# Kernel tuning notes

Measured on AMD Instinct MI355X. Metric: run time of the kernel, lower is better.

The kernel has to match this reference:

```python
import jax, jax.numpy as jnp
import numpy as np

D_MODEL = 1024
NUM_HEADS = 16
HEAD_DIM = D_MODEL // NUM_HEADS
THETA = 10000.0
MAX_SEQ_LEN = 2048
BATCH = 4
SEQ = 2048


def _rope_tables():
    # theta_vec = 1 / theta**(arange(0, d_k, 2)/d_k), pos outer product
    inv_freq = 1.0 / (THETA ** (jnp.arange(0, HEAD_DIM, 2, dtype=jnp.float32) / HEAD_DIM))
    pos = jnp.arange(MAX_SEQ_LEN, dtype=jnp.float32)
    freqs = jnp.outer(pos, inv_freq)  # [max_seq, head_dim//2]
    return jnp.cos(freqs), jnp.sin(freqs)


def apply_rope(x, cos, sin):
    # x: [..., S, d]; cos/sin: [S, d//2]; interleaved pairwise rotation
    x1 = x[..., 0::2]
    x2 = x[..., 1::2]
    o1 = x1 * cos - x2 * sin
    o2 = x2 * cos + x1 * sin
    return jnp.stack([o1, o2], axis=-1).reshape(x.shape)


def setup_inputs() -> dict:
    key = jax.random.key(0)
    kx, kq, kk, kv, ko = jax.random.split(key, 5)
    std = (1.0 / D_MODEL) ** 0.5
    x = jax.random.normal(kx, (BATCH, SEQ, D_MODEL), dtype=jnp.float32)
    w_q = jax.random.normal(kq, (D_MODEL, D_MODEL), dtype=jnp.float32) * std
    w_k = jax.random.normal(kk, (D_MODEL, D_MODEL), dtype=jnp.float32) * std
    w_v = jax.random.normal(kv, (D_MODEL, D_MODEL), dtype=jnp.float32) * std
    w_o = jax.random.normal(ko, (D_MODEL, D_MODEL), dtype=jnp.float32) * std
    cos, sin = _rope_tables()
    return {"x": x, "w_q": w_q, "w_k": w_k, "w_v": w_v, "w_o": w_o,
            "cos": cos, "sin": sin}


def reference(x, w_q, w_k, w_v, w_o, cos, sin):
    b, s, d = x.shape
    h, dk = NUM_HEADS, HEAD_DIM

    def proj(w):
        # einsum '... s d, hd d -> ... s hd' == x @ w.T, then split heads
        y = jnp.einsum('bsd,ed->bse', x, w)
        return y.reshape(b, s, h, dk).transpose(0, 2, 1, 3)  # [b,h,s,dk]

    q = apply_rope(proj(w_q), cos[:s], sin[:s])
    k = apply_rope(proj(w_k), cos[:s], sin[:s])
    v = proj(w_v)

    scores = jnp.einsum('bhnd,bhmd->bhnm', q, k) / (dk ** 0.5)
    causal = jnp.tril(jnp.ones((s, s), dtype=bool))
    scores = jnp.where(causal, scores, -jnp.inf)
    attn = jax.nn.softmax(scores, axis=-1)
    out = jnp.einsum('bhnm,bhmd->bhnd', attn, v)  # [b,h,s,dk]
    out = out.transpose(0, 2, 1, 3).reshape(b, s, d)
    # einsum '... s hd, d hd -> ... s d' == out @ w_o.T
    return jnp.einsum('bse,de->bsd', out, w_o)
```

## Files before the change

### kernel.cpp

```cpp
#include <hip/hip_runtime.h>
#include <hip/hip_bf16.h>


typedef __bf16 bf16;
typedef __bf16 bf16x8 __attribute__((ext_vector_type(8)));
typedef __bf16 bf16x4 __attribute__((ext_vector_type(4)));
typedef float f32x4 __attribute__((ext_vector_type(4)));

#define LOG2E 1.4426950408889634f
#define QSCALE (0.125f * LOG2E * 8388608.0f)
#define SEXP_SEED ((126.94269504f - 16.0f * LOG2E) * 8388608.0f)

__device__ __forceinline__ void async16(const void* g, void* l) {
  __builtin_amdgcn_global_load_lds(
      (const __attribute__((address_space(1))) void*)g,
      (__attribute__((address_space(3))) void*)l, 16, 0, 0);
}

#define MFMA16(a, b, c) __builtin_amdgcn_mfma_f32_16x16x32_bf16(a, b, c, 0, 0, 0)

__global__ void cast_all_kernel(const float* __restrict__ x,
                                const float* __restrict__ wq,
                                const float* __restrict__ wk,
                                const float* __restrict__ wv,
                                const float* __restrict__ wo,
                                const float* __restrict__ cosT,
                                const float* __restrict__ sinT,
                                bf16* __restrict__ xb, bf16* __restrict__ wb,
                                float2* __restrict__ csT) {
  int i = blockIdx.x * blockDim.x + threadIdx.x;
  if (i >= 3145728) {
    int j = i - 3145728;
    float2 cs;
    cs.x = cosT[j];
    cs.y = sinT[j];
    csT[j] = cs;
    return;
  }
  const float* src;
  bf16* dst;
  long o;
  if (i < 2097152) {
    src = x; dst = xb; o = i;
  } else {
    long j = i - 2097152;
    int w = (int)(j >> 18);
    o = j & 262143;
    src = (w == 0) ? wq : (w == 1) ? wk : (w == 2) ? wv : wo;
    dst = wb + (long)w * 1048576;
  }
  float4 v = reinterpret_cast<const float4*>(src)[o];
  bf16x4 out;
  out.x = (bf16)v.x; out.y = (bf16)v.y; out.z = (bf16)v.z; out.w = (bf16)v.w;
  *reinterpret_cast<bf16x4*>(dst + o * 4) = out;
}

template <int EPI, int TM, int TN>
__device__ __forceinline__ void gemm_dev(const bf16* __restrict__ A,
                                         const bf16* __restrict__ B,
                                         void* __restrict__ C, int N, int K,
                                         int bm, int bn, bf16* As, bf16* Bs,
                                         const float2* __restrict__ csT) {
  constexpr int WM = TM / 64;
  constexpr int WN = 4 / WM;
  constexpr int CW = TN / WN;
  constexpr int NT = CW / 16;
  constexpr int ROUNDS = (TM + TN) / 32;
  const int tid = threadIdx.x;
  const int wid = tid >> 6, lane = tid & 63;
  const int quad = lane >> 4, l15 = lane & 15;
  const int waveM = wid / WN, waveN = wid % WN;

  f32x4 acc[4][NT] = {};
  const bf16* Ag = A + (long)bm * TM * K;
  const bf16* Bg = B + (long)bn * TN * K;

  for (int k0 = 0; k0 < K; k0 += 64) {
#pragma unroll
    for (int ri = 0; ri < ROUNDS; ++ri) {
      int ci = ri * 256 + tid;
      int gb = ri * 256 + (wid << 6);
      bool isA = gb < TM * 8;
      int cl = isA ? ci : ci - TM * 8;
      int r = cl >> 3;
      int col = ((cl & 7) ^ (r & 7)) << 3;
      const bf16* src = (isA ? Ag : Bg) + (long)r * K + k0 + col;
      char* dst = isA ? ((char*)As + (long)ci * 16)
                      : ((char*)Bs + (long)(ci - TM * 8) * 16);
      async16(src, dst);
    }
    __syncthreads();
#pragma unroll
    for (int kk = 0; kk < 2; ++kk) {
      bf16x8 af[4], bfr[NT];
#pragma unroll
      for (int t = 0; t < 4; ++t) {
        int rowA = waveM * 64 + t * 16 + l15;
        af[t] = *(const bf16x8*)(As + rowA * 64 +
                                 ((((kk << 2) + quad) ^ (rowA & 7)) << 3));
      }
#pragma unroll
      for (int t = 0; t < NT; ++t) {
        int rowB = waveN * CW + t * 16 + l15;
        bfr[t] = *(const bf16x8*)(Bs + rowB * 64 +
                                  ((((kk << 2) + quad) ^ (rowB & 7)) << 3));
      }
#pragma unroll
      for (int mt = 0; mt < 4; ++mt)
#pragma unroll
        for (int nt = 0; nt < NT; ++nt)
          acc[mt][nt] = MFMA16(af[mt], bfr[nt], acc[mt][nt]);
    }
    if (k0 + 64 < K) __syncthreads();
  }

  const float qsc = (EPI == 0 && bn < 8) ? QSCALE : 1.0f;
#pragma unroll
  for (int mt = 0; mt < 4; ++mt)
#pragma unroll
    for (int nt = 0; nt < NT; ++nt)
#pragma unroll
      for (int r = 0; r < 4; ++r) {
        int row = bm * TM + waveM * 64 + mt * 16 + quad * 4 + r;
        int col = bn * TN + waveN * CW + nt * 16 + l15;
        float v = acc[mt][nt][r];
        if (EPI == 0) {
          float pr = __shfl_xor(v, 1);
          int d = col & 63;
          float2 cs = csT[(row & 2047) * 32 + (d >> 1)];
          float o =
              (col & 1) ? (v * cs.x + pr * cs.y) : (v * cs.x - pr * cs.y);
          o *= qsc;
          long off = (long)(col >> 10) * 8388608 +
                     (long)(((row >> 11) << 4) + ((col >> 6) & 15)) * 131072 +
                     (long)(row & 2047) * 64 + d;
          ((bf16*)C)[off] = (bf16)o;
        } else if (EPI == 1) {
          long off = (long)(col >> 11) * 2097152 + (long)row * 2048 +
                     (col & 2047);
          ((bf16*)C)[off] = (bf16)v;
        } else {
          ((float*)C)[(long)row * N + col] = v;
        }
      }
}

__global__ __launch_bounds__(256) void gemm_qkv(const bf16* __restrict__ xb,
                                                const bf16* __restrict__ wqk,
                                                const bf16* __restrict__ wv,
                                                bf16* __restrict__ QK,
                                                bf16* __restrict__ VT,
                                                const float2* __restrict__ csT) {
  __shared__ __align__(16) bf16 As[128 * 64];
  __shared__ __align__(16) bf16 Bs[128 * 64];
  int p = blockIdx.x;
  if (p >= 1024) {
    int pv = p - 1024;
    int lv = (pv & 7) * 64 + (pv >> 3);
    gemm_dev<1, 128, 128>(wv, xb, VT, 8192, 1024, lv & 7, lv >> 3, As, Bs,
                          nullptr);
  } else {
    int l = (p & 7) * 128 + (p >> 3);
    gemm_dev<0, 128, 128>(xb, wqk, QK, 2048, 1024, l >> 4, l & 15, As, Bs,
                          csT);
  }
}

__global__ __launch_bounds__(256) void gemm_out(const bf16* __restrict__ A,
                                                const bf16* __restrict__ B,
                                                float* __restrict__ C) {
  __shared__ __align__(16) bf16 As[128 * 64];
  __shared__ __align__(16) bf16 Bs[128 * 64];
  int p = blockIdx.x;
  int l = (p & 7) * 64 + (p >> 3);
  gemm_dev<2, 128, 128>(A, B, C, 1024, 1024, l >> 3, l & 7, As, Bs, nullptr);
}

__device__ __forceinline__ void attn_step(const bf16* Ks, const bf16* Vs,
                                          bf16* Pw, const bf16x8* qf,
                                          const bf16x8 ones, f32x4* accO,
                                          f32x4& accL, int quad, int l15,
                                          int qloc, bool diag) {
  const int sw = l15 & 7;
  const f32x4 seedv = {SEXP_SEED, SEXP_SEED, SEXP_SEED, SEXP_SEED};
  f32x4 sacc[4] = {seedv, seedv, seedv, seedv};
#pragma unroll
  for (int mt = 0; mt < 4; ++mt)
#pragma unroll
    for (int kk = 0; kk < 2; ++kk) {
      bf16x8 kf = *(const bf16x8*)(Ks + (mt * 16 + l15) * 64 +
                                   ((((kk << 2) + quad) ^ sw) << 3));
      sacc[mt] = MFMA16(kf, qf[kk], sacc[mt]);
    }
  if (diag) {
#pragma unroll
    for (int mt = 0; mt < 4; ++mt)
#pragma unroll
      for (int r = 0; r < 4; ++r)
        if ((mt * 16 + quad * 4 + r) > qloc) sacc[mt][r] = 0.0f;
  }
#pragma unroll
  for (int mt = 0; mt < 4; ++mt) {
    int i0 = (int)sacc[mt][0], i1 = (int)sacc[mt][1];
    int i2 = (int)sacc[mt][2], i3 = (int)sacc[mt][3];
    uint2 pk;
    pk.x = __builtin_amdgcn_perm((unsigned)i1, (unsigned)i0, 0x07060302u);
    pk.y = __builtin_amdgcn_perm((unsigned)i3, (unsigned)i2, 0x07060302u);
    *(uint2*)(Pw + l15 * 88 + mt * 16 + quad * 4) = pk;
  }
  asm volatile("s_waitcnt lgkmcnt(0)" ::: "memory");
  bf16x8 pfr[2];
#pragma unroll
  for (int kk = 0; kk < 2; ++kk)
    pfr[kk] = *(const bf16x8*)(Pw + l15 * 88 + kk * 32 + quad * 8);
#pragma unroll
  for (int nt = 0; nt < 4; ++nt)
#pragma unroll
    for (int kk = 0; kk < 2; ++kk) {
      bf16x8 vf = *(const bf16x8*)(Vs + (nt * 16 + l15) * 64 +
                                   ((((kk << 2) + quad) ^ sw) << 3));
      accO[nt] = MFMA16(pfr[kk], vf, accO[nt]);
    }
#pragma unroll
  for (int kk = 0; kk < 2; ++kk)
    accL = MFMA16(pfr[kk], ones, accL);
}

__global__ __launch_bounds__(256, 4) void attn_kernel(
    const bf16* __restrict__ Q, const bf16* __restrict__ Kg,
    const bf16* __restrict__ VT, bf16* __restrict__ Out) {
  __shared__ __align__(16) bf16 Ks[64 * 64];
  __shared__ __align__(16) bf16 Vs[64 * 64];
  __shared__ __align__(16) bf16 Ps[4][16 * 88];
  const int tid = threadIdx.x, wid = tid >> 6, lane = tid & 63;
  const int quad = lane >> 4, l15 = lane & 15;
  const int id = blockIdx.x;
  const int p = (id >> 3) & 15;
  const int bh = (id & 7) * 8 + (id >> 7);
  const int q0t = p, q1t = 31 - p;
  const bf16* Qb = Q + (long)bh * 131072;
  const bf16* Kb = Kg + (long)bh * 131072;
  const bf16* Vb = VT + (long)bh * 131072;
  bf16* Pw = &Ps[wid][0];
  const int qloc = wid * 16 + l15;

  bf16x8 ones;
#pragma unroll
  for (int j = 0; j < 8; ++j) ones[j] = (bf16)1.0f;

  bf16x8 qf0[2], qf1[2];
#pragma unroll
  for (int kk = 0; kk < 2; ++kk) {
    qf0[kk] = *(const bf16x8*)(Qb + (long)(q0t * 64 + qloc) * 64 + kk * 32 +
                               quad * 8);
    qf1[kk] = *(const bf16x8*)(Qb + (long)(q1t * 64 + qloc) * 64 + kk * 32 +
                               quad * 8);
  }
  f32x4 acc0[4] = {}, acc1[4] = {};
  f32x4 accL0 = {}, accL1 = {};

  for (int kt = 0; kt <= q1t; ++kt) {
#pragma unroll
    for (int it = 0; it < 2; ++it) {
      int chunk = it * 256 + tid;
      int r = chunk >> 3;
      int c = (((chunk & 7) ^ (r & 7)) << 3);
      int ldsbase = (it * 256 + wid * 64) * 16;
      async16(Kb + (long)(kt * 64 + r) * 64 + c, (char*)Ks + ldsbase);
      async16(Vb + (long)r * 2048 + kt * 64 + c, (char*)Vs + ldsbase);
    }
    __syncthreads();
    attn_step(Ks, Vs, Pw, qf1, ones, acc1, accL1, quad, l15, qloc, kt == q1t);
    if (kt <= q0t)
      attn_step(Ks, Vs, Pw, qf0, ones, acc0, accL0, quad, l15, qloc,
                kt == q0t);
    __syncthreads();
  }

  const int b = bh >> 4, h = bh & 15;
#pragma unroll
  for (int r = 0; r < 4; ++r) {
    float lr0 = 1.0f / accL0[r];
    float lr1 = 1.0f / accL1[r];
#pragma unroll
    for (int nt = 0; nt < 4; ++nt) {
      int d = h * 64 + nt * 16 + l15;
      int qg0 = q0t * 64 + wid * 16 + quad * 4 + r;
      int qg1 = q1t * 64 + wid * 16 + quad * 4 + r;
      Out[(long)(b * 2048 + qg0) * 1024 + d] = (bf16)(acc0[nt][r] * lr0);
      Out[(long)(b * 2048 + qg1) * 1024 + d] = (bf16)(acc1[nt][r] * lr1);
    }
  }
}

extern "C" void kernel_launch(void* const* d_in, const int* in_sizes, int n_in,
                              void* d_out, int out_size, void* d_ws,
                              size_t ws_size, hipStream_t stream) {
  const float* x = (const float*)d_in[0];
  const float* w_q = (const float*)d_in[1];
  const float* w_k = (const float*)d_in[2];
  const float* w_v = (const float*)d_in[3];
  const float* w_o = (const float*)d_in[4];
  const float* cosT = (const float*)d_in[5];
  const float* sinT = (const float*)d_in[6];

  char* ws = (char*)d_ws;
  bf16* xb = (bf16*)(ws + 0);
  bf16* wqb = (bf16*)(ws + 16777216);
  bf16* wvb = (bf16*)(ws + 20971520);
  bf16* wob = (bf16*)(ws + 23068672);
  bf16* Qb = (bf16*)(ws + 25165824);
  bf16* Kb = (bf16*)(ws + 41943040);
  bf16* VTb = (bf16*)(ws + 58720256);
  float2* csT = (float2*)(ws + 75497472);
  bf16* attnb = xb;

  cast_all_kernel<<<12544, 256, 0, stream>>>(x, w_q, w_k, w_v, w_o, cosT,
                                             sinT, xb, wqb, csT);

  gemm_qkv<<<1536, 256, 0, stream>>>(xb, wqb, wvb, Qb, VTb, csT);

  attn_kernel<<<1024, 256, 0, stream>>>(Qb, Kb, VTb, attnb);

  gemm_out<<<512, 256, 0, stream>>>(attnb, wob, (float*)d_out);
}
```

Baseline: 235.7 us.

## Split-K output GEMM with atomics and interleave two query tiles in attention

The output projection GEMM now splits K into two halves across twice as many blocks, accumulating into a zeroed fp32 output with atomicAdd. Its aim is better occupancy on a 512-block launch. The attention kernel gains a fused step that processes both query tiles per K/V tile, sharing K/V fragment loads and interleaving independent MFMA chains, with a separate P buffer per tile. The costs are an extra memset, atomic traffic, extra LDS and more register pressure.

```diff
diff --git a/kernel.cpp b/kernel.cpp
--- a/kernel.cpp
+++ b/kernel.cpp
@@ -59,7 +59,8 @@
 __device__ __forceinline__ void gemm_dev(const bf16* __restrict__ A,
                                          const bf16* __restrict__ B,
                                          void* __restrict__ C, int N, int K,
-                                         int bm, int bn, bf16* As, bf16* Bs,
+                                         int ldk, int bm, int bn, bf16* As,
+                                         bf16* Bs,
                                          const float2* __restrict__ csT) {
   constexpr int WM = TM / 64;
   constexpr int WN = 4 / WM;
@@ -72,8 +73,8 @@
   const int waveM = wid / WN, waveN = wid % WN;
 
   f32x4 acc[4][NT] = {};
-  const bf16* Ag = A + (long)bm * TM * K;
-  const bf16* Bg = B + (long)bn * TN * K;
+  const bf16* Ag = A + (long)bm * TM * ldk;
+  const bf16* Bg = B + (long)bn * TN * ldk;
 
   for (int k0 = 0; k0 < K; k0 += 64) {
 #pragma unroll
@@ -84,7 +85,7 @@
       int cl = isA ? ci : ci - TM * 8;
       int r = cl >> 3;
       int col = ((cl & 7) ^ (r & 7)) << 3;
-      const bf16* src = (isA ? Ag : Bg) + (long)r * K + k0 + col;
+      const bf16* src = (isA ? Ag : Bg) + (long)r * ldk + k0 + col;
       char* dst = isA ? ((char*)As + (long)ci * 16)
                       : ((char*)Bs + (long)(ci - TM * 8) * 16);
       async16(src, dst);
@@ -139,8 +140,10 @@
           long off = (long)(col >> 11) * 2097152 + (long)row * 2048 +
                      (col & 2047);
           ((bf16*)C)[off] = (bf16)v;
+        } else if (EPI == 2) {
+          ((float*)C)[(long)row * N + col] = v;
         } else {
-          ((float*)C)[(long)row * N + col] = v;
+          atomicAdd(&((float*)C)[(long)row * N + col], v);
         }
       }
 }
@@ -157,12 +160,12 @@
   if (p >= 1024) {
     int pv = p - 1024;
     int lv = (pv & 7) * 64 + (pv >> 3);
-    gemm_dev<1, 128, 128>(wv, xb, VT, 8192, 1024, lv & 7, lv >> 3, As, Bs,
-                          nullptr);
+    gemm_dev<1, 128, 128>(wv, xb, VT, 8192, 1024, 1024, lv & 7, lv >> 3, As,
+                          Bs, nullptr);
   } else {
     int l = (p & 7) * 128 + (p >> 3);
-    gemm_dev<0, 128, 128>(xb, wqk, QK, 2048, 1024, l >> 4, l & 15, As, Bs,
-                          csT);
+    gemm_dev<0, 128, 128>(xb, wqk, QK, 2048, 1024, 1024, l >> 4, l & 15, As,
+                          Bs, csT);
   }
 }
 
@@ -172,8 +175,20 @@
   __shared__ __align__(16) bf16 As[128 * 64];
   __shared__ __align__(16) bf16 Bs[128 * 64];
   int p = blockIdx.x;
-  int l = (p & 7) * 64 + (p >> 3);
-  gemm_dev<2, 128, 128>(A, B, C, 1024, 1024, l >> 3, l & 7, As, Bs, nullptr);
+  int kh = p >> 9;
+  int t = p & 511;
+  int l = (t & 7) * 64 + (t >> 3);
+  gemm_dev<3, 128, 128>(A + kh * 512, B + kh * 512, C, 1024, 512, 1024,
+                        l >> 3, l & 7, As, Bs, nullptr);
+}
+
+__device__ __forceinline__ void pack_row(const f32x4& s, bf16* Pw, int l15,
+                                         int mt, int quad) {
+  int i0 = (int)s[0], i1 = (int)s[1], i2 = (int)s[2], i3 = (int)s[3];
+  uint2 pk;
+  pk.x = __builtin_amdgcn_perm((unsigned)i1, (unsigned)i0, 0x07060302u);
+  pk.y = __builtin_amdgcn_perm((unsigned)i3, (unsigned)i2, 0x07060302u);
+  *(uint2*)(Pw + l15 * 88 + mt * 16 + quad * 4) = pk;
 }
 
 __device__ __forceinline__ void attn_step(const bf16* Ks, const bf16* Vs,
@@ -183,30 +198,21 @@
                                           int qloc, bool diag) {
   const int sw = l15 & 7;
   const f32x4 seedv = {SEXP_SEED, SEXP_SEED, SEXP_SEED, SEXP_SEED};
-  f32x4 sacc[4] = {seedv, seedv, seedv, seedv};
-#pragma unroll
-  for (int mt = 0; mt < 4; ++mt)
+#pragma unroll
+  for (int mt = 0; mt < 4; ++mt) {
+    f32x4 s = seedv;
 #pragma unroll
     for (int kk = 0; kk < 2; ++kk) {
       bf16x8 kf = *(const bf16x8*)(Ks + (mt * 16 + l15) * 64 +
                                    ((((kk << 2) + quad) ^ sw) << 3));
-      sacc[mt] = MFMA16(kf, qf[kk], sacc[mt]);
-    }
-  if (diag) {
-#pragma unroll
-    for (int mt = 0; mt < 4; ++mt)
+      s = MFMA16(kf, qf[kk], s);
+    }
+    if (diag) {
 #pragma unroll
       for (int r = 0; r < 4; ++r)
-        if ((mt * 16 + quad * 4 + r) > qloc) sacc[mt][r] = 0.0f;
-  }
-#pragma unroll
-  for (int mt = 0; mt < 4; ++mt) {
-    int i0 = (int)sacc[mt][0], i1 = (int)sacc[mt][1];
-    int i2 = (int)sacc[mt][2], i3 = (int)sacc[mt][3];
-    uint2 pk;
-    pk.x = __builtin_amdgcn_perm((unsigned)i1, (unsigned)i0, 0x07060302u);
-    pk.y = __builtin_amdgcn_perm((unsigned)i3, (unsigned)i2, 0x07060302u);
-    *(uint2*)(Pw + l15 * 88 + mt * 16 + quad * 4) = pk;
+        if ((mt * 16 + quad * 4 + r) > qloc) s[r] = 0.0f;
+    }
+    pack_row(s, Pw, l15, mt, quad);
   }
   asm volatile("s_waitcnt lgkmcnt(0)" ::: "memory");
   bf16x8 pfr[2];
@@ -224,6 +230,53 @@
 #pragma unroll
   for (int kk = 0; kk < 2; ++kk)
     accL = MFMA16(pfr[kk], ones, accL);
+}
+
+__device__ __forceinline__ void attn_step2(
+    const bf16* Ks, const bf16* Vs, bf16* Pw1, bf16* Pw0, const bf16x8* qf1,
+    const bf16x8* qf0, const bf16x8 ones, f32x4* acc1, f32x4* acc0,
+    f32x4& accL1, f32x4& accL0, int quad, int l15, int qloc, bool diag0) {
+  const int sw = l15 & 7;
+  const f32x4 seedv = {SEXP_SEED, SEXP_SEED, SEXP_SEED, SEXP_SEED};
+#pragma unroll
+  for (int mt = 0; mt < 4; ++mt) {
+    f32x4 s1 = seedv, s0 = seedv;
+#pragma unroll
+    for (int kk = 0; kk < 2; ++kk) {
+      bf16x8 kf = *(const bf16x8*)(Ks + (mt * 16 + l15) * 64 +
+                                   ((((kk << 2) + quad) ^ sw) << 3));
+      s1 = MFMA16(kf, qf1[kk], s1);
+      s0 = MFMA16(kf, qf0[kk], s0);
+    }
+    if (diag0) {
+#pragma unroll
+      for (int r = 0; r < 4; ++r)
+        if ((mt * 16 + quad * 4 + r) > qloc) s0[r] = 0.0f;
+    }
+    pack_row(s1, Pw1, l15, mt, quad);
+    pack_row(s0, Pw0, l15, mt, quad);
+  }
+  asm volatile("s_waitcnt lgkmcnt(0)" ::: "memory");
+  bf16x8 pf1[2], pf0[2];
+#pragma unroll
+  for (int kk = 0; kk < 2; ++kk) {
+    pf1[kk] = *(const bf16x8*)(Pw1 + l15 * 88 + kk * 32 + quad * 8);
+    pf0[kk] = *(const bf16x8*)(Pw0 + l15 * 88 + kk * 32 + quad * 8);
+  }
+#pragma unroll
+  for (int nt = 0; nt < 4; ++nt)
+#pragma unroll
+    for (int kk = 0; kk < 2; ++kk) {
+      bf16x8 vf = *(const bf16x8*)(Vs + (nt * 16 + l15) * 64 +
+                                   ((((kk << 2) + quad) ^ sw) << 3));
+      acc1[nt] = MFMA16(pf1[kk], vf, acc1[nt]);
+      acc0[nt] = MFMA16(pf0[kk], vf, acc0[nt]);
+    }
+#pragma unroll
+  for (int kk = 0; kk < 2; ++kk) {
+    accL1 = MFMA16(pf1[kk], ones, accL1);
+    accL0 = MFMA16(pf0[kk], ones, accL0);
+  }
 }
 
 __global__ __launch_bounds__(256, 4) void attn_kernel(
@@ -231,7 +284,7 @@
     const bf16* __restrict__ VT, bf16* __restrict__ Out) {
   __shared__ __align__(16) bf16 Ks[64 * 64];
   __shared__ __align__(16) bf16 Vs[64 * 64];
-  __shared__ __align__(16) bf16 Ps[4][16 * 88];
+  __shared__ __align__(16) bf16 Ps[4][2][16 * 88];
   const int tid = threadIdx.x, wid = tid >> 6, lane = tid & 63;
   const int quad = lane >> 4, l15 = lane & 15;
   const int id = blockIdx.x;
@@ -241,7 +294,8 @@
   const bf16* Qb = Q + (long)bh * 131072;
   const bf16* Kb = Kg + (long)bh * 131072;
   const bf16* Vb = VT + (long)bh * 131072;
-  bf16* Pw = &Ps[wid][0];
+  bf16* Pw1 = &Ps[wid][0][0];
+  bf16* Pw0 = &Ps[wid][1][0];
   const int qloc = wid * 16 + l15;
 
   bf16x8 ones;
@@ -270,10 +324,12 @@
       async16(Vb + (long)r * 2048 + kt * 64 + c, (char*)Vs + ldsbase);
     }
     __syncthreads();
-    attn_step(Ks, Vs, Pw, qf1, ones, acc1, accL1, quad, l15, qloc, kt == q1t);
     if (kt <= q0t)
-      attn_step(Ks, Vs, Pw, qf0, ones, acc0, accL0, quad, l15, qloc,
-                kt == q0t);
+      attn_step2(Ks, Vs, Pw1, Pw0, qf1, qf0, ones, acc1, acc0, accL1, accL0,
+                 quad, l15, qloc, kt == q0t);
+    else
+      attn_step(Ks, Vs, Pw1, qf1, ones, acc1, accL1, quad, l15, qloc,
+                kt == q1t);
     __syncthreads();
   }
 
@@ -318,9 +374,11 @@
   cast_all_kernel<<<12544, 256, 0, stream>>>(x, w_q, w_k, w_v, w_o, cosT,
                                              sinT, xb, wqb, csT);
 
+  hipMemsetAsync(d_out, 0, (size_t)out_size, stream);
+
   gemm_qkv<<<1536, 256, 0, stream>>>(xb, wqb, wvb, Qb, VTb, csT);
 
   attn_kernel<<<1024, 256, 0, stream>>>(Qb, Kb, VTb, attnb);
 
-  gemm_out<<<512, 256, 0, stream>>>(attnb, wob, (float*)d_out);
-}
+  gemm_out<<<1024, 256, 0, stream>>>(attnb, wob, (float*)d_out);
+}
```

Result: slower. 286.3 us (+21.5%).

## Split paired causal q-tiles into one q-tile per block, longest first

Applied to the files above, without the earlier changes.

Replaces the paired-tile scheme, where each block handled q-tiles p and 31-p together for balance, with one q-tile per block and twice as many blocks. Blocks are ordered so the longest causal tiles launch first, leaving the LPT-style scheduler to balance the load. This halves per-block accumulator registers and may raise occupancy. In exchange, K/V tiles are no longer shared between two query tiles, so K/V traffic from global memory rises.

```diff
diff --git a/kernel.cpp b/kernel.cpp
--- a/kernel.cpp
+++ b/kernel.cpp
@@ -235,9 +235,9 @@
   const int tid = threadIdx.x, wid = tid >> 6, lane = tid & 63;
   const int quad = lane >> 4, l15 = lane & 15;
   const int id = blockIdx.x;
-  const int p = (id >> 3) & 15;
-  const int bh = (id & 7) * 8 + (id >> 7);
-  const int q0t = p, q1t = 31 - p;
+  const int local = id >> 3;
+  const int bh = (id & 7) * 8 + (local & 7);
+  const int qt = 31 - (local >> 3);
   const bf16* Qb = Q + (long)bh * 131072;
   const bf16* Kb = Kg + (long)bh * 131072;
   const bf16* Vb = VT + (long)bh * 131072;
@@ -248,18 +248,15 @@
 #pragma unroll
   for (int j = 0; j < 8; ++j) ones[j] = (bf16)1.0f;
 
-  bf16x8 qf0[2], qf1[2];
-#pragma unroll
-  for (int kk = 0; kk < 2; ++kk) {
-    qf0[kk] = *(const bf16x8*)(Qb + (long)(q0t * 64 + qloc) * 64 + kk * 32 +
-                               quad * 8);
-    qf1[kk] = *(const bf16x8*)(Qb + (long)(q1t * 64 + qloc) * 64 + kk * 32 +
-                               quad * 8);
-  }
-  f32x4 acc0[4] = {}, acc1[4] = {};
-  f32x4 accL0 = {}, accL1 = {};
-
-  for (int kt = 0; kt <= q1t; ++kt) {
+  bf16x8 qf[2];
+#pragma unroll
+  for (int kk = 0; kk < 2; ++kk)
+    qf[kk] = *(const bf16x8*)(Qb + (long)(qt * 64 + qloc) * 64 + kk * 32 +
+                              quad * 8);
+  f32x4 acc[4] = {};
+  f32x4 accL = {};
+
+  for (int kt = 0; kt <= qt; ++kt) {
 #pragma unroll
     for (int it = 0; it < 2; ++it) {
       int chunk = it * 256 + tid;
@@ -270,25 +267,19 @@
       async16(Vb + (long)r * 2048 + kt * 64 + c, (char*)Vs + ldsbase);
     }
     __syncthreads();
-    attn_step(Ks, Vs, Pw, qf1, ones, acc1, accL1, quad, l15, qloc, kt == q1t);
-    if (kt <= q0t)
-      attn_step(Ks, Vs, Pw, qf0, ones, acc0, accL0, quad, l15, qloc,
-                kt == q0t);
+    attn_step(Ks, Vs, Pw, qf, ones, acc, accL, quad, l15, qloc, kt == qt);
     __syncthreads();
   }
 
   const int b = bh >> 4, h = bh & 15;
 #pragma unroll
   for (int r = 0; r < 4; ++r) {
-    float lr0 = 1.0f / accL0[r];
-    float lr1 = 1.0f / accL1[r];
+    float lr = 1.0f / accL[r];
 #pragma unroll
     for (int nt = 0; nt < 4; ++nt) {
       int d = h * 64 + nt * 16 + l15;
-      int qg0 = q0t * 64 + wid * 16 + quad * 4 + r;
-      int qg1 = q1t * 64 + wid * 16 + quad * 4 + r;
-      Out[(long)(b * 2048 + qg0) * 1024 + d] = (bf16)(acc0[nt][r] * lr0);
-      Out[(long)(b * 2048 + qg1) * 1024 + d] = (bf16)(acc1[nt][r] * lr1);
+      int qg = qt * 64 + wid * 16 + quad * 4 + r;
+      Out[(long)(b * 2048 + qg) * 1024 + d] = (bf16)(acc[nt][r] * lr);
     }
   }
 }
@@ -320,7 +311,7 @@
 
   gemm_qkv<<<1536, 256, 0, stream>>>(xb, wqb, wvb, Qb, VTb, csT);
 
-  attn_kernel<<<1024, 256, 0, stream>>>(Qb, Kb, VTb, attnb);
+  attn_kernel<<<2048, 256, 0, stream>>>(Qb, Kb, VTb, attnb);
 
   gemm_out<<<512, 256, 0, stream>>>(attnb, wob, (float*)d_out);
 }
```

Measured after the change: 236.5 us. No clear change (+0.3%).
